# Optimization experiments

Measured on AMD Instinct MI355X. Metric: run time of the kernel, lower is better.

Reference implementation:

```python
import jax, jax.numpy as jnp
import numpy as np

INV_SQRT2 = 0.7071067811865476  # 1/sqrt(2), haar filter coefficient
LEVEL = 2
EFF = 3          # effective modes per axis: (16 // omega=6) + 1
OUT_C = 64
SUBBANDS = ("aad", "ada", "add", "daa", "dad", "dda", "ddd")


def dwt1(x, axis):
    # Haar analysis along `axis` (even length, periodic => no padding needed).
    x = jnp.moveaxis(x, axis, -1)
    e, o = x[..., ::2], x[..., 1::2]
    a = (e + o) * INV_SQRT2
    d = (e - o) * INV_SQRT2
    return jnp.moveaxis(a, -1, axis), jnp.moveaxis(d, -1, axis)


def idwt1(a, d, axis):
    a = jnp.moveaxis(a, axis, -1)
    d = jnp.moveaxis(d, axis, -1)
    e = (a + d) * INV_SQRT2
    o = (a - d) * INV_SQRT2
    x = jnp.stack([e, o], axis=-1).reshape(e.shape[:-1] + (2 * e.shape[-1],))
    return jnp.moveaxis(x, -1, axis)


def dwt3(x):
    # One level of separable 3D DWT over last 3 axes -> dict of 8 subbands.
    ax, dx = dwt1(x, -3)
    out = {}
    for nx, tx in (("a", ax), ("d", dx)):
        ay, dy = dwt1(tx, -2)
        for ny, ty in (("a", ay), ("d", dy)):
            az, dz = dwt1(ty, -1)
            out[nx + ny + "a"] = az
            out[nx + ny + "d"] = dz
    return out


def idwt3(c):
    aa = idwt1(c["aaa"], c["aad"], -1)
    ad = idwt1(c["ada"], c["add"], -1)
    da = idwt1(c["daa"], c["dad"], -1)
    dd = idwt1(c["dda"], c["ddd"], -1)
    a = idwt1(aa, ad, -2)
    d = idwt1(da, dd, -2)
    return idwt1(a, d, -3)


def spectralconv(waves, w4):
    # waves: [B, Ci, X, Y, Z] real; w4: [4, Ci, Co, m, m, m] complex.
    B, Ci, X, Y, Z = waves.shape
    m = EFF
    xw = jnp.fft.rfftn(waves, axes=(-3, -2, -1))
    out = jnp.zeros((B, OUT_C, X, Y, Z // 2 + 1), dtype=xw.dtype)
    mul = lambda blk, w: jnp.einsum("bixyz,ioxyz->boxyz", blk, w)
    out = out.at[:, :, :m, :m, :m].set(mul(xw[:, :, :m, :m, :m], w4[0]))
    out = out.at[:, :, -m:, :m, :m].set(mul(xw[:, :, -m:, :m, :m], w4[1]))
    out = out.at[:, :, :m, -m:, :m].set(mul(xw[:, :, :m, -m:, :m], w4[2]))
    out = out.at[:, :, -m:, -m:, :m].set(mul(xw[:, :, -m:, -m:, :m], w4[3]))
    return jnp.fft.irfftn(out, s=(X, Y, Z), axes=(-3, -2, -1))


def _forward(x, weights):
    # weights: [8, 4, Ci, Co, m, m, m, 2] real -> complex [8, 4, Ci, Co, m, m, m]
    w = jax.lax.complex(weights[..., 0], weights[..., 1])
    # multi-level wavedec3: details[0] = finest, details[-1] = coarsest
    a = x
    details = []
    for _ in range(LEVEL):
        c = dwt3(a)
        a = c.pop("aaa")
        details.append(c)
    # spectral conv on coarsest approx + 7 coarsest detail subbands
    a = spectralconv(a, w[0])
    coarse = details[-1]
    details[-1] = {k: spectralconv(coarse[k], w[i + 1]) for i, k in enumerate(SUBBANDS)}
    # waverec3
    for c in reversed(details):
        full = dict(c)
        full["aaa"] = a
        a = idwt3(full)
    return a


def setup_inputs() -> dict:
    key = jax.random.key(0)
    kx, kw = jax.random.split(key)
    x = jax.random.normal(kx, (4, 64, 64, 64, 64), dtype=jnp.float32)
    scale = 1.0 / (64 * 64)
    weights = scale * jax.random.uniform(kw, (8, 4, 64, 64, 3, 3, 3, 2), dtype=jnp.float32)
    return {"x": x, "weights": weights}


def reference(x, weights):
    return _forward(x, weights)
```

## Files before the change

### kernel.cpp

```cpp
#include <hip/hip_runtime.h>


typedef float f32x4 __attribute__((ext_vector_type(4)));
typedef float f32x2 __attribute__((ext_vector_type(2)));

__constant__ float C16c[16] = {
  1.0f, 0.92387953251128675f, 0.70710678118654752f, 0.38268343236508977f,
  0.0f, -0.38268343236508977f, -0.70710678118654752f, -0.92387953251128675f,
  -1.0f, -0.92387953251128675f, -0.70710678118654752f, -0.38268343236508977f,
  0.0f, 0.38268343236508977f, 0.70710678118654752f, 0.92387953251128675f
};
__constant__ float S16c[16] = {
  0.0f, 0.38268343236508977f, 0.70710678118654752f, 0.92387953251128675f,
  1.0f, 0.92387953251128675f, 0.70710678118654752f, 0.38268343236508977f,
  0.0f, -0.38268343236508977f, -0.70710678118654752f, -0.92387953251128675f,
  -1.0f, -0.92387953251128675f, -0.70710678118654752f, -0.38268343236508977f
};
__constant__ int KYv[6] = {0, 1, 2, 13, 14, 15};

__global__ __launch_bounds__(256) void k1_front_wtr(const float* __restrict__ x,
                                                    const float2* __restrict__ w2,
                                                    float2* __restrict__ g2,
                                                    float2* __restrict__ wt) {
  __shared__ __align__(16) unsigned char smem[13824];
  unsigned tid = threadIdx.x;
  if (blockIdx.x < 4096u) {
    float* sm = (float*)smem;
    float2* fz = (float2*)(smem + 8704);
    unsigned px = blockIdx.x & 15u;
    unsigned bc = blockIdx.x >> 4;
    const f32x4* xp4 = (const f32x4*)(x + ((size_t)bc << 18)) + (size_t)px * 4096u;
    unsigned z4 = tid & 15u;
#pragma unroll
    for (int q = 0; q < 4; q++) {
      float a00 = 0.f, a01 = 0.f, a10 = 0.f, a11 = 0.f;
#pragma unroll
      for (int i = 0; i < 4; i++) {
        f32x4 v = xp4[i * 1024 + q * 256 + tid];
        float h0 = v.x + v.y, h1 = v.z + v.w;
        a00 += h0; a01 += h1;
        if (i < 2) { a10 += h0; a11 += h1; } else { a10 -= h0; a11 -= h1; }
      }
      float p00 = a00 + __shfl_xor(a00, 16);
      float p01 = a01 + __shfl_xor(a01, 16);
      float p10 = a10 + __shfl_xor(a10, 16);
      float p11 = a11 + __shfl_xor(a11, 16);
      float q00 = __shfl_xor(p00, 32), q01 = __shfl_xor(p01, 32);
      float q10 = __shfl_xor(p10, 32), q11 = __shfl_xor(p11, 32);
      bool hi = (tid >> 5) & 1u;
      float ya0 = p00 + q00, yd0 = hi ? (q00 - p00) : (p00 - q00);
      float ya1 = p01 + q01, yd1 = hi ? (q01 - p01) : (p01 - q01);
      float za0 = p10 + q10, zd0 = hi ? (q10 - p10) : (p10 - q10);
      float za1 = p11 + q11, zd1 = hi ? (q11 - p11) : (p11 - q11);
      if (((tid >> 4) & 3u) == 0u) {
        unsigned py = q * 4 + (tid >> 6);
        float* smp = sm + py * 17u + z4;
        smp[0 * 272] = (ya0 + ya1) * 0.125f;
        smp[1 * 272] = (ya0 - ya1) * 0.125f;
        smp[2 * 272] = (yd0 + yd1) * 0.125f;
        smp[3 * 272] = (yd0 - yd1) * 0.125f;
        smp[4 * 272] = (za0 + za1) * 0.125f;
        smp[5 * 272] = (za0 - za1) * 0.125f;
        smp[6 * 272] = (zd0 + zd1) * 0.125f;
        smp[7 * 272] = (zd0 - zd1) * 0.125f;
      }
    }
    __syncthreads();
    if (tid < 128u) {
      unsigned k = tid >> 4, y = tid & 15u;
      const float* row = sm + k * 272u + y * 17u;
#pragma unroll
      for (int kz = 0; kz < 3; kz++) {
        float re = 0.f, im = 0.f;
#pragma unroll
        for (int nz = 0; nz < 16; nz++) {
          float vv = row[nz];
          int t16 = (kz * nz) & 15;
          re += vv * C16c[t16];
          im -= vv * S16c[t16];
        }
        fz[k * 51u + kz * 17u + y] = make_float2(re, im);
      }
    }
    __syncthreads();
    if (tid < 144u) {
      unsigned k = tid / 18u, r = tid - k * 18u;
      unsigned kyi = r / 3u, kz = r - kyi * 3u;
      int ky = KYv[kyi];
      float re = 0.f, im = 0.f;
#pragma unroll
      for (int ny = 0; ny < 16; ny++) {
        float2 vv = fz[k * 51u + kz * 17u + ny];
        int t16 = (ky * ny) & 15;
        float c = C16c[t16], sn = S16c[t16];
        re += vv.x * c + vv.y * sn;
        im += vv.y * c - vv.x * sn;
      }
      g2[((size_t)tid * 16u + px) * 256u + bc] = make_float2(re, im);
    }
  } else {
    f32x4* lw4 = (f32x4*)smem;
    float2* lw2 = (float2*)smem;
    unsigned wb = blockIdx.x - 4096u;
    unsigned kc = wb >> 6, i = wb & 63u;
    const f32x4* src = (const f32x4*)(w2 + ((size_t)kc * 64u + i) * 1728u);
    for (unsigned t = tid; t < 864u; t += 256u) lw4[t] = src[t];
    __syncthreads();
    float2* dst = wt + (size_t)kc * 110592u + (size_t)i * 64u;
    for (unsigned t = tid; t < 1728u; t += 256u) {
      unsigned f = t >> 6, o = t & 63u;
      dst[(size_t)f * 4096u + o] = lw2[o * 27u + f];
    }
  }
}

__global__ __launch_bounds__(256) void k2_mix(const float2* __restrict__ wt,
                                              const float2* __restrict__ g2,
                                              float2* __restrict__ oh2) {
  __shared__ float2 inl[256];
  unsigned tid = threadIdx.x;
  unsigned f = blockIdx.x % 27u;
  unsigned kc = blockIdx.x / 27u;
  unsigned k = kc >> 2, corner = kc & 3u;
  unsigned kz = f % 3u, kyl = (f / 3u) % 3u, kxl = f / 9u;
  unsigned kxi = kxl + 3u * (corner & 1u);
  unsigned kyi = kyl + 3u * (corner >> 1);
  unsigned fg = kxi * 18u + kyi * 3u + kz;
  unsigned row = k * 18u + kyi * 3u + kz;
  {
    const float2* gp = g2 + (size_t)row * 4096u + tid;
    int kx = KYv[kxi];
    float re = 0.f, im = 0.f;
#pragma unroll
    for (int nx = 0; nx < 16; nx++) {
      float2 vv = gp[nx * 256];
      int t16 = (kx * nx) & 15;
      float c = C16c[t16], sn = S16c[t16];
      re += vv.x * c + vv.y * sn;
      im += vv.y * c - vv.x * sn;
    }
    inl[tid] = make_float2(re, im);
  }
  __syncthreads();
  unsigned b = tid >> 6, o = tid & 63u;
  const f32x2* wp = (const f32x2*)(wt + ((size_t)kc * 27u + f) * 4096u + o);
  float2 acc = make_float2(0.f, 0.f);
#pragma unroll 16
  for (unsigned i = 0; i < 64u; i++) {
    float2 a = inl[(b << 6) | i];
    f32x2 ww = __builtin_nontemporal_load(wp + (size_t)i * 64u);
    acc.x += a.x * ww.x - a.y * ww.y;
    acc.y += a.x * ww.y + a.y * ww.x;
  }
  oh2[((size_t)(b * 64u + o)) * 864u + k * 108u + fg] = acc;
}

__global__ __launch_bounds__(256) void k3_invsynth(const float2* __restrict__ oh2,
                                                   const float* __restrict__ x,
                                                   float* __restrict__ out) {
  __shared__ float2 hh[864];
  __shared__ float2 gx[2][8][18];
  __shared__ float2 uu[2][8][3][16];
  __shared__ float W[2][8][16][16];
  unsigned tid = threadIdx.x;
  unsigned sp = blockIdx.x & 7u;
  unsigned bo = 255u - (blockIdx.x >> 3);
  for (unsigned i = tid; i < 864u; i += 256u)
    hh[i] = oh2[(size_t)bo * 864u + i];
  __syncthreads();
  for (unsigned i = tid; i < 288u; i += 256u) {
    unsigned sl = i / 144u, j = i - sl * 144u;
    unsigned k = j / 18u, r = j - k * 18u;
    unsigned nx = sp * 2u + sl;
    float re = 0.f, im = 0.f;
#pragma unroll
    for (int kxi = 0; kxi < 6; kxi++) {
      float2 v = hh[k * 108u + kxi * 18 + r];
      int t16 = (KYv[kxi] * (int)nx) & 15;
      float c = C16c[t16], sn = S16c[t16];
      re += v.x * c - v.y * sn;
      im += v.x * sn + v.y * c;
    }
    gx[sl][k][r] = make_float2(re, im);
  }
  __syncthreads();
  for (unsigned i = tid; i < 768u; i += 256u) {
    unsigned sl = i / 384u, j = i - sl * 384u;
    unsigned k = j / 48u, rem = j - k * 48u;
    unsigned kz = rem >> 4, ny = rem & 15u;
    float re = 0.f, im = 0.f;
#pragma unroll
    for (int kyi = 0; kyi < 6; kyi++) {
      float2 v = gx[sl][k][kyi * 3 + kz];
      int t16 = (KYv[kyi] * (int)ny) & 15;
      float c = C16c[t16], sn = S16c[t16];
      re += v.x * c - v.y * sn;
      im += v.x * sn + v.y * c;
    }
    uu[sl][k][kz][ny] = make_float2(re, im);
  }
  __syncthreads();
  for (unsigned i = tid; i < 512u; i += 256u) {
    unsigned sl = i >> 8, ny = (i >> 4) & 15u, nz = i & 15u;
    float c1 = C16c[nz], s1 = S16c[nz];
    int t2 = (2 * nz) & 15;
    float c2 = C16c[t2], s2 = S16c[t2];
    float val[8];
#pragma unroll
    for (int k = 0; k < 8; k++) {
      float2 u0 = uu[sl][k][0][ny], u1 = uu[sl][k][1][ny], u2 = uu[sl][k][2][ny];
      val[k] = (u0.x + 2.f * (u1.x * c1 - u1.y * s1) + 2.f * (u2.x * c2 - u2.y * s2)) * (1.f / 4096.f);
    }
#pragma unroll
    for (int st = 1; st < 8; st <<= 1)
#pragma unroll
      for (int i2 = 0; i2 < 8; i2++)
        if (!(i2 & st)) {
          float a = val[i2], b = val[i2 | st];
          val[i2] = a + b;
          val[i2 | st] = a - b;
        }
#pragma unroll
    for (int m = 0; m < 8; m++) W[sl][m][ny][nz] = val[m];
  }
  __syncthreads();
  unsigned w = tid >> 6, l = tid & 63u;
  unsigned z4 = l & 15u, y2 = l >> 4;
  unsigned mmy = ((y2 >> 1) & 1u) << 1;
  const float* xp = x + ((size_t)bo << 18);
  float* op = out + ((size_t)bo << 18);
#pragma unroll
  for (unsigned sl = 0; sl < 2u; ++sl) {
#pragma unroll
    for (unsigned r2 = 0; r2 < 8u; ++r2) {
      unsigned xp2 = r2 & 1u, yg = r2 >> 1;
      unsigned X0 = ((sp * 2u + sl) << 2) + (xp2 << 1);
      unsigned Y = (yg << 4) + (w << 2) + y2;
      size_t off = ((size_t)X0 << 12) + (Y << 6) + (z4 << 2);
      f32x4 v0 = __builtin_nontemporal_load((const f32x4*)(xp + off));
      f32x4 v1 = __builtin_nontemporal_load((const f32x4*)(xp + off + 4096u));
      float h0 = v0.x + v0.y + v1.x + v1.y;
      float h1 = v0.z + v0.w + v1.z + v1.w;
      float m0 = (h0 + __shfl_xor(h0, 16)) * 0.125f;
      float m1 = (h1 + __shfl_xor(h1, 16)) * 0.125f;
      unsigned ny = (yg << 2) + w;
      unsigned mm = (xp2 << 2) | mmy;
      float c0 = 0.125f * W[sl][mm][ny][z4] - m0;
      float c1 = 0.125f * W[sl][mm | 1u][ny][z4] - m1;
      v0.x += c0; v0.y += c0; v0.z += c1; v0.w += c1;
      v1.x += c0; v1.y += c0; v1.z += c1; v1.w += c1;
      __builtin_nontemporal_store(v0, (f32x4*)(op + off));
      __builtin_nontemporal_store(v1, (f32x4*)(op + off + 4096u));
    }
  }
}

extern "C" void kernel_launch(void* const* d_in, const int* in_sizes, int n_in,
                              void* d_out, int out_size, void* d_ws, size_t ws_size,
                              hipStream_t stream) {
  const float* x = (const float*)d_in[0];
  const float* w = (const float*)d_in[1];
  float* out = (float*)d_out;

  const size_t G_F2 = 144ull * 4096;
  const size_t WT_F2 = 32ull * 27 * 4096;
  const size_t OH_F2 = 256ull * 864;
  const size_t G_B = G_F2 * 8, WT_B = WT_F2 * 8, OH_B = OH_F2 * 8;

  float2 *g2, *wt, *oh2;
  char* ws = (char*)d_ws;
  if (ws_size >= G_B + WT_B + OH_B) {
    g2 = (float2*)ws;
    wt = (float2*)(ws + G_B);
    oh2 = (float2*)(ws + G_B + WT_B);
  } else {
    g2 = (float2*)d_out;
    wt = (float2*)((char*)d_out + G_B);
    oh2 = (float2*)ws;
  }

  k1_front_wtr<<<6144, 256, 0, stream>>>(x, (const float2*)w, g2, wt);
  k2_mix<<<864, 256, 0, stream>>>(wt, g2, oh2);
  k3_invsynth<<<2048, 256, 0, stream>>>(oh2, x, out);
}
```

Baseline: 167.5 us.

## Drop weight transpose pass; read raw weights in mix kernel with batched accumulation

The separate weight-transpose blocks in the front kernel are removed. The mix kernel now reads the original complex weight layout directly and reuses each weight across all four batches. The g2 layout is changed to [b][row][nx][c] so that the x-axis DFT inputs load coalesced, and each mix block computes all 27 frequencies for its corner into shared memory. The last kernel switches from nontemporal to normal loads of x. The trade-offs are fewer mix blocks (256, 216 active threads in the weight phase), strided 4-byte weight loads, and redundant x-DFT work repeated across the 8 output-channel blocks.

```diff
diff --git a/kernel.cpp b/kernel.cpp
--- a/kernel.cpp
+++ b/kernel.cpp
@@ -2,7 +2,6 @@
 
 
 typedef float f32x4 __attribute__((ext_vector_type(4)));
-typedef float f32x2 __attribute__((ext_vector_type(2)));
 
 __constant__ float C16c[16] = {
   1.0f, 0.92387953251128675f, 0.70710678118654752f, 0.38268343236508977f,
@@ -18,141 +17,144 @@
 };
 __constant__ int KYv[6] = {0, 1, 2, 13, 14, 15};
 
-__global__ __launch_bounds__(256) void k1_front_wtr(const float* __restrict__ x,
-                                                    const float2* __restrict__ w2,
-                                                    float2* __restrict__ g2,
-                                                    float2* __restrict__ wt) {
-  __shared__ __align__(16) unsigned char smem[13824];
+__global__ __launch_bounds__(256) void k1_front(const float* __restrict__ x,
+                                                float2* __restrict__ g2) {
+  __shared__ float sm[8 * 16 * 17 + 8];
+  __shared__ float2 fz[8 * 3 * 17];
   unsigned tid = threadIdx.x;
-  if (blockIdx.x < 4096u) {
-    float* sm = (float*)smem;
-    float2* fz = (float2*)(smem + 8704);
-    unsigned px = blockIdx.x & 15u;
-    unsigned bc = blockIdx.x >> 4;
-    const f32x4* xp4 = (const f32x4*)(x + ((size_t)bc << 18)) + (size_t)px * 4096u;
-    unsigned z4 = tid & 15u;
-#pragma unroll
-    for (int q = 0; q < 4; q++) {
-      float a00 = 0.f, a01 = 0.f, a10 = 0.f, a11 = 0.f;
-#pragma unroll
-      for (int i = 0; i < 4; i++) {
-        f32x4 v = xp4[i * 1024 + q * 256 + tid];
-        float h0 = v.x + v.y, h1 = v.z + v.w;
-        a00 += h0; a01 += h1;
-        if (i < 2) { a10 += h0; a11 += h1; } else { a10 -= h0; a11 -= h1; }
+  unsigned px = blockIdx.x & 15u;
+  unsigned bc = blockIdx.x >> 4;
+  unsigned c = bc & 63u, b = bc >> 6;
+  const f32x4* xp4 = (const f32x4*)(x + ((size_t)bc << 18)) + (size_t)px * 4096u;
+  unsigned z4 = tid & 15u;
+#pragma unroll
+  for (int q = 0; q < 4; q++) {
+    float a00 = 0.f, a01 = 0.f, a10 = 0.f, a11 = 0.f;
+#pragma unroll
+    for (int i = 0; i < 4; i++) {
+      f32x4 v = xp4[i * 1024 + q * 256 + tid];
+      float h0 = v.x + v.y, h1 = v.z + v.w;
+      a00 += h0; a01 += h1;
+      if (i < 2) { a10 += h0; a11 += h1; } else { a10 -= h0; a11 -= h1; }
+    }
+    float p00 = a00 + __shfl_xor(a00, 16);
+    float p01 = a01 + __shfl_xor(a01, 16);
+    float p10 = a10 + __shfl_xor(a10, 16);
+    float p11 = a11 + __shfl_xor(a11, 16);
+    float q00 = __shfl_xor(p00, 32), q01 = __shfl_xor(p01, 32);
+    float q10 = __shfl_xor(p10, 32), q11 = __shfl_xor(p11, 32);
+    bool hi = (tid >> 5) & 1u;
+    float ya0 = p00 + q00, yd0 = hi ? (q00 - p00) : (p00 - q00);
+    float ya1 = p01 + q01, yd1 = hi ? (q01 - p01) : (p01 - q01);
+    float za0 = p10 + q10, zd0 = hi ? (q10 - p10) : (p10 - q10);
+    float za1 = p11 + q11, zd1 = hi ? (q11 - p11) : (p11 - q11);
+    if (((tid >> 4) & 3u) == 0u) {
+      unsigned py = q * 4 + (tid >> 6);
+      float* smp = sm + py * 17u + z4;
+      smp[0 * 272] = (ya0 + ya1) * 0.125f;
+      smp[1 * 272] = (ya0 - ya1) * 0.125f;
+      smp[2 * 272] = (yd0 + yd1) * 0.125f;
+      smp[3 * 272] = (yd0 - yd1) * 0.125f;
+      smp[4 * 272] = (za0 + za1) * 0.125f;
+      smp[5 * 272] = (za0 - za1) * 0.125f;
+      smp[6 * 272] = (zd0 + zd1) * 0.125f;
+      smp[7 * 272] = (zd0 - zd1) * 0.125f;
+    }
+  }
+  __syncthreads();
+  if (tid < 128u) {
+    unsigned k = tid >> 4, y = tid & 15u;
+    const float* row = sm + k * 272u + y * 17u;
+#pragma unroll
+    for (int kz = 0; kz < 3; kz++) {
+      float re = 0.f, im = 0.f;
+#pragma unroll
+      for (int nz = 0; nz < 16; nz++) {
+        float vv = row[nz];
+        int t16 = (kz * nz) & 15;
+        re += vv * C16c[t16];
+        im -= vv * S16c[t16];
       }
-      float p00 = a00 + __shfl_xor(a00, 16);
-      float p01 = a01 + __shfl_xor(a01, 16);
-      float p10 = a10 + __shfl_xor(a10, 16);
-      float p11 = a11 + __shfl_xor(a11, 16);
-      float q00 = __shfl_xor(p00, 32), q01 = __shfl_xor(p01, 32);
-      float q10 = __shfl_xor(p10, 32), q11 = __shfl_xor(p11, 32);
-      bool hi = (tid >> 5) & 1u;
-      float ya0 = p00 + q00, yd0 = hi ? (q00 - p00) : (p00 - q00);
-      float ya1 = p01 + q01, yd1 = hi ? (q01 - p01) : (p01 - q01);
-      float za0 = p10 + q10, zd0 = hi ? (q10 - p10) : (p10 - q10);
-      float za1 = p11 + q11, zd1 = hi ? (q11 - p11) : (p11 - q11);
-      if (((tid >> 4) & 3u) == 0u) {
-        unsigned py = q * 4 + (tid >> 6);
-        float* smp = sm + py * 17u + z4;
-        smp[0 * 272] = (ya0 + ya1) * 0.125f;
-        smp[1 * 272] = (ya0 - ya1) * 0.125f;
-        smp[2 * 272] = (yd0 + yd1) * 0.125f;
-        smp[3 * 272] = (yd0 - yd1) * 0.125f;
-        smp[4 * 272] = (za0 + za1) * 0.125f;
-        smp[5 * 272] = (za0 - za1) * 0.125f;
-        smp[6 * 272] = (zd0 + zd1) * 0.125f;
-        smp[7 * 272] = (zd0 - zd1) * 0.125f;
-      }
-    }
-    __syncthreads();
-    if (tid < 128u) {
-      unsigned k = tid >> 4, y = tid & 15u;
-      const float* row = sm + k * 272u + y * 17u;
-#pragma unroll
-      for (int kz = 0; kz < 3; kz++) {
-        float re = 0.f, im = 0.f;
-#pragma unroll
-        for (int nz = 0; nz < 16; nz++) {
-          float vv = row[nz];
-          int t16 = (kz * nz) & 15;
-          re += vv * C16c[t16];
-          im -= vv * S16c[t16];
-        }
-        fz[k * 51u + kz * 17u + y] = make_float2(re, im);
-      }
-    }
-    __syncthreads();
-    if (tid < 144u) {
-      unsigned k = tid / 18u, r = tid - k * 18u;
-      unsigned kyi = r / 3u, kz = r - kyi * 3u;
-      int ky = KYv[kyi];
-      float re = 0.f, im = 0.f;
-#pragma unroll
-      for (int ny = 0; ny < 16; ny++) {
-        float2 vv = fz[k * 51u + kz * 17u + ny];
-        int t16 = (ky * ny) & 15;
-        float c = C16c[t16], sn = S16c[t16];
-        re += vv.x * c + vv.y * sn;
-        im += vv.y * c - vv.x * sn;
-      }
-      g2[((size_t)tid * 16u + px) * 256u + bc] = make_float2(re, im);
-    }
-  } else {
-    f32x4* lw4 = (f32x4*)smem;
-    float2* lw2 = (float2*)smem;
-    unsigned wb = blockIdx.x - 4096u;
-    unsigned kc = wb >> 6, i = wb & 63u;
-    const f32x4* src = (const f32x4*)(w2 + ((size_t)kc * 64u + i) * 1728u);
-    for (unsigned t = tid; t < 864u; t += 256u) lw4[t] = src[t];
-    __syncthreads();
-    float2* dst = wt + (size_t)kc * 110592u + (size_t)i * 64u;
-    for (unsigned t = tid; t < 1728u; t += 256u) {
-      unsigned f = t >> 6, o = t & 63u;
-      dst[(size_t)f * 4096u + o] = lw2[o * 27u + f];
-    }
-  }
-}
-
-__global__ __launch_bounds__(256) void k2_mix(const float2* __restrict__ wt,
+      fz[k * 51u + kz * 17u + y] = make_float2(re, im);
+    }
+  }
+  __syncthreads();
+  if (tid < 144u) {
+    unsigned k = tid / 18u, r = tid - k * 18u;
+    unsigned kyi = r / 3u, kz = r - kyi * 3u;
+    int ky = KYv[kyi];
+    float re = 0.f, im = 0.f;
+#pragma unroll
+    for (int ny = 0; ny < 16; ny++) {
+      float2 vv = fz[k * 51u + kz * 17u + ny];
+      int t16 = (ky * ny) & 15;
+      float cc = C16c[t16], sn = S16c[t16];
+      re += vv.x * cc + vv.y * sn;
+      im += vv.y * cc - vv.x * sn;
+    }
+    g2[(((size_t)b * 144u + tid) * 16u + px) * 64u + c] = make_float2(re, im);
+  }
+}
+
+__global__ __launch_bounds__(256) void k2_mix(const float* __restrict__ w2,
                                               const float2* __restrict__ g2,
                                               float2* __restrict__ oh2) {
-  __shared__ float2 inl[256];
+  __shared__ float2 ihl[4][64][27];
   unsigned tid = threadIdx.x;
-  unsigned f = blockIdx.x % 27u;
-  unsigned kc = blockIdx.x / 27u;
+  unsigned kc = blockIdx.x >> 3;
+  unsigned ob = blockIdx.x & 7u;
   unsigned k = kc >> 2, corner = kc & 3u;
-  unsigned kz = f % 3u, kyl = (f / 3u) % 3u, kxl = f / 9u;
-  unsigned kxi = kxl + 3u * (corner & 1u);
-  unsigned kyi = kyl + 3u * (corner >> 1);
-  unsigned fg = kxi * 18u + kyi * 3u + kz;
-  unsigned row = k * 18u + kyi * 3u + kz;
+  unsigned kxi0 = 3u * (corner & 1u), kyi0 = 3u * (corner >> 1);
   {
-    const float2* gp = g2 + (size_t)row * 4096u + tid;
-    int kx = KYv[kxi];
-    float re = 0.f, im = 0.f;
-#pragma unroll
-    for (int nx = 0; nx < 16; nx++) {
-      float2 vv = gp[nx * 256];
-      int t16 = (kx * nx) & 15;
-      float c = C16c[t16], sn = S16c[t16];
-      re += vv.x * c + vv.y * sn;
-      im += vv.y * c - vv.x * sn;
-    }
-    inl[tid] = make_float2(re, im);
-  }
-  __syncthreads();
-  unsigned b = tid >> 6, o = tid & 63u;
-  const f32x2* wp = (const f32x2*)(wt + ((size_t)kc * 27u + f) * 4096u + o);
-  float2 acc = make_float2(0.f, 0.f);
-#pragma unroll 16
+    unsigned c = tid & 63u, b = tid >> 6;
+    const float2* gb = g2 + ((size_t)b * 144u * 16u) * 64u + c;
+#pragma unroll
+    for (unsigned kyl = 0; kyl < 3u; kyl++) {
+#pragma unroll
+      for (unsigned kz = 0; kz < 3u; kz++) {
+        unsigned row = k * 18u + (kyl + kyi0) * 3u + kz;
+        float2 rg[16];
+#pragma unroll
+        for (int nx = 0; nx < 16; nx++) rg[nx] = gb[((size_t)row * 16u + nx) * 64u];
+#pragma unroll
+        for (unsigned kxl = 0; kxl < 3u; kxl++) {
+          int kx = KYv[kxl + kxi0];
+          float re = 0.f, im = 0.f;
+#pragma unroll
+          for (int nx = 0; nx < 16; nx++) {
+            int t16 = (kx * nx) & 15;
+            float cc = C16c[t16], sn = S16c[t16];
+            re += rg[nx].x * cc + rg[nx].y * sn;
+            im += rg[nx].y * cc - rg[nx].x * sn;
+          }
+          ihl[b][c][kxl * 9u + kyl * 3u + kz] = make_float2(re, im);
+        }
+      }
+    }
+  }
+  __syncthreads();
+  if (tid >= 216u) return;
+  unsigned o = tid / 27u, f = tid - o * 27u;
+  const float* wp = w2 + (((size_t)kc * 64u * 64u + (ob * 8u + o)) * 27u + f) * 2u;
+  float2 acc[4];
+#pragma unroll
+  for (int b = 0; b < 4; b++) acc[b] = make_float2(0.f, 0.f);
+#pragma unroll 8
   for (unsigned i = 0; i < 64u; i++) {
-    float2 a = inl[(b << 6) | i];
-    f32x2 ww = __builtin_nontemporal_load(wp + (size_t)i * 64u);
-    acc.x += a.x * ww.x - a.y * ww.y;
-    acc.y += a.x * ww.y + a.y * ww.x;
-  }
-  oh2[((size_t)(b * 64u + o)) * 864u + k * 108u + fg] = acc;
+    float wr = __builtin_nontemporal_load(wp + (size_t)i * 3456u);
+    float wi = __builtin_nontemporal_load(wp + (size_t)i * 3456u + 1u);
+#pragma unroll
+    for (int b = 0; b < 4; b++) {
+      float2 a = ihl[b][i][f];
+      acc[b].x += a.x * wr - a.y * wi;
+      acc[b].y += a.x * wi + a.y * wr;
+    }
+  }
+  unsigned kxl = f / 9u, kyl = (f - kxl * 9u) / 3u, kz = f % 3u;
+  unsigned fg = (kxl + kxi0) * 18u + (kyl + kyi0) * 3u + kz;
+#pragma unroll
+  for (int b = 0; b < 4; b++)
+    oh2[((size_t)(b * 64u + ob * 8u + o)) * 864u + k * 108u + fg] = acc[b];
 }
 
 __global__ __launch_bounds__(256) void k3_invsynth(const float2* __restrict__ oh2,
@@ -177,9 +179,9 @@
     for (int kxi = 0; kxi < 6; kxi++) {
       float2 v = hh[k * 108u + kxi * 18 + r];
       int t16 = (KYv[kxi] * (int)nx) & 15;
-      float c = C16c[t16], sn = S16c[t16];
-      re += v.x * c - v.y * sn;
-      im += v.x * sn + v.y * c;
+      float cc = C16c[t16], sn = S16c[t16];
+      re += v.x * cc - v.y * sn;
+      im += v.x * sn + v.y * cc;
     }
     gx[sl][k][r] = make_float2(re, im);
   }
@@ -193,9 +195,9 @@
     for (int kyi = 0; kyi < 6; kyi++) {
       float2 v = gx[sl][k][kyi * 3 + kz];
       int t16 = (KYv[kyi] * (int)ny) & 15;
-      float c = C16c[t16], sn = S16c[t16];
-      re += v.x * c - v.y * sn;
-      im += v.x * sn + v.y * c;
+      float cc = C16c[t16], sn = S16c[t16];
+      re += v.x * cc - v.y * sn;
+      im += v.x * sn + v.y * cc;
     }
     uu[sl][k][kz][ny] = make_float2(re, im);
   }
@@ -216,9 +218,9 @@
 #pragma unroll
       for (int i2 = 0; i2 < 8; i2++)
         if (!(i2 & st)) {
-          float a = val[i2], b = val[i2 | st];
-          val[i2] = a + b;
-          val[i2 | st] = a - b;
+          float a = val[i2], bb = val[i2 | st];
+          val[i2] = a + bb;
+          val[i2 | st] = a - bb;
         }
 #pragma unroll
     for (int m = 0; m < 8; m++) W[sl][m][ny][nz] = val[m];
@@ -237,8 +239,8 @@
       unsigned X0 = ((sp * 2u + sl) << 2) + (xp2 << 1);
       unsigned Y = (yg << 4) + (w << 2) + y2;
       size_t off = ((size_t)X0 << 12) + (Y << 6) + (z4 << 2);
-      f32x4 v0 = __builtin_nontemporal_load((const f32x4*)(xp + off));
-      f32x4 v1 = __builtin_nontemporal_load((const f32x4*)(xp + off + 4096u));
+      f32x4 v0 = *(const f32x4*)(xp + off);
+      f32x4 v1 = *(const f32x4*)(xp + off + 4096u);
       float h0 = v0.x + v0.y + v1.x + v1.y;
       float h1 = v0.z + v0.w + v1.z + v1.w;
       float m0 = (h0 + __shfl_xor(h0, 16)) * 0.125f;
@@ -262,24 +264,20 @@
   const float* w = (const float*)d_in[1];
   float* out = (float*)d_out;
 
-  const size_t G_F2 = 144ull * 4096;
-  const size_t WT_F2 = 32ull * 27 * 4096;
-  const size_t OH_F2 = 256ull * 864;
-  const size_t G_B = G_F2 * 8, WT_B = WT_F2 * 8, OH_B = OH_F2 * 8;
-
-  float2 *g2, *wt, *oh2;
+  const size_t G_B = 4ull * 144 * 16 * 64 * 8;
+  const size_t OH_B = 256ull * 864 * 8;
+
+  float2 *g2, *oh2;
   char* ws = (char*)d_ws;
-  if (ws_size >= G_B + WT_B + OH_B) {
+  if (ws_size >= G_B + OH_B) {
     g2 = (float2*)ws;
-    wt = (float2*)(ws + G_B);
-    oh2 = (float2*)(ws + G_B + WT_B);
+    oh2 = (float2*)(ws + G_B);
   } else {
-    g2 = (float2*)d_out;
-    wt = (float2*)((char*)d_out + G_B);
     oh2 = (float2*)ws;
-  }
-
-  k1_front_wtr<<<6144, 256, 0, stream>>>(x, (const float2*)w, g2, wt);
-  k2_mix<<<864, 256, 0, stream>>>(wt, g2, oh2);
+    g2 = (float2*)((char*)d_out + (size_t)out_size * 4 - G_B);
+  }
+
+  k1_front<<<4096, 256, 0, stream>>>(x, g2);
+  k2_mix<<<256, 256, 0, stream>>>(w, g2, oh2);
   k3_invsynth<<<2048, 256, 0, stream>>>(oh2, x, out);
 }
```

Result: faster. 154.9 us (-7.5%).
